# Optimization experiments

Measured on AMD Instinct MI355X. Metric: run time of the kernel, lower is better.

Reference implementation:

```python
import jax, jax.numpy as jnp
import numpy as np

SURR_SCALE = 10.0  # AbstractSNNLayer.surr_scale
THRESH = 0.3       # inf_th=False

@jax.custom_vjp
def spike_fn(x):
    # ActFunFastSigmoid.forward: heaviside
    return (x > 0).astype(x.dtype)

def _spike_fwd(x):
    return spike_fn(x), x

def _spike_bwd(x, g):
    # fast-sigmoid surrogate: g / (scale*|x| + 1)^2
    return (g / (SURR_SCALE * jnp.abs(x) + 1.0) ** 2,)

spike_fn.defvjp(_spike_fwd, _spike_bwd)


def setup_inputs() -> dict:
    B, NIN, NOUT = 1024, 4096, 4096
    key = jax.random.key(0)
    k1, k2, k3, k4, k5 = jax.random.split(key, 5)
    prev_spikes = jax.random.bernoulli(k1, 0.2, (B, NIN)).astype(jnp.float32)
    own_mems = 0.1 * jax.random.normal(k2, (B, NOUT), dtype=jnp.float32)
    own_spikes = jax.random.bernoulli(k3, 0.2, (B, NOUT)).astype(jnp.float32)
    W = jax.random.normal(k4, (NOUT, NIN), dtype=jnp.float32) / np.sqrt(NIN)
    tau_m = jax.random.normal(k5, (NOUT,), dtype=jnp.float32)
    return {"prev_spikes": prev_spikes, "own_mems": own_mems,
            "own_spikes": own_spikes, "W": W, "tau_m": tau_m}


def reference(prev_spikes, own_mems, own_spikes, W, tau_m):
    # update_mem: mem = mem * sigmoid(tau_m) * (1 - o_spike) + Linear(i_spike)
    alpha = jax.nn.sigmoid(tau_m)                      # [NOUT]
    mem = own_mems * alpha * (1.0 - own_spikes) \
          + jnp.einsum('bi,oi->bo', prev_spikes, W)    # [B, NOUT]
    # activation_function: spike with surrogate grad, then reset-to-zero
    o_spike = spike_fn(mem - THRESH)
    mem = jnp.where(mem < THRESH, mem, 0.0)            # mem * (mem < th_reset)
    return mem, o_spike
```

## Files before the change

### kernel.cpp

```cpp
#include <hip/hip_runtime.h>
#include <stdint.h>

#define NB 1024
#define NK 4096
#define NO 4096
#define DELTA 4e-7

typedef __attribute__((ext_vector_type(8))) short s16x8;
typedef __attribute__((ext_vector_type(4))) float f32x4;
typedef __attribute__((ext_vector_type(4))) int i32x4;
typedef __attribute__((ext_vector_type(16))) char c8x16;

static __device__ __forceinline__ unsigned short f2bf_rne(float x) {
  union { float f; unsigned u; } c; c.f = x;
  unsigned r = (c.u + 0x7FFFu + ((c.u >> 16) & 1u)) >> 16;
  return (unsigned short)r;
}
static __device__ __forceinline__ float bf2f(unsigned short h) {
  union { float f; unsigned u; } c; c.u = ((unsigned)h) << 16;
  return c.f;
}

static __device__ __forceinline__ void gload16(const void* g, void* l) {
  __builtin_amdgcn_global_load_lds((const __attribute__((address_space(1))) void*)g,
                                   (__attribute__((address_space(3))) void*)l, 16, 0, 0);
}

__global__ void cvtA8t_kernel(const float* __restrict__ A, signed char* __restrict__ A8t) {
  const int n = NB * NK / 16;
  for (int i = blockIdx.x * blockDim.x + threadIdx.x; i < n; i += gridDim.x * blockDim.x) {
    const int bm = i >> 15, rem = i & 32767;
    const int kt = rem >> 9, rem2 = rem & 511;
    const int l = rem2 >> 3, c = rem2 & 7;
    const int row = bm * 128 + 2 * l + (c >> 2);
    const int col = kt * 64 + (c & 3) * 16;
    const float* src = A + ((size_t)row << 12) + col;
    c8x16 v;
#pragma unroll
    for (int j = 0; j < 4; ++j) {
      float4 f = *(const float4*)(src + j * 4);
      v[j * 4 + 0] = (char)(int)f.x; v[j * 4 + 1] = (char)(int)f.y;
      v[j * 4 + 2] = (char)(int)f.z; v[j * 4 + 3] = (char)(int)f.w;
    }
    const size_t dst = ((size_t)(bm * 64 + kt) << 13) + l * 128 + ((c ^ (l & 7)) << 4);
    *(c8x16*)(A8t + dst) = v;
  }
}

__global__ void cvtW8t_kernel(const float* __restrict__ W, signed char* __restrict__ W8t) {
  const int n = NO * NK / 16;
  for (int i = blockIdx.x * blockDim.x + threadIdx.x; i < n; i += gridDim.x * blockDim.x) {
    const int bn = i >> 14, rem = i & 16383;
    const int kt = rem >> 8, rem2 = rem & 255;
    const int l = rem2 >> 3, c = rem2 & 7;
    const int row = bn * 64 + 2 * l + (c >> 2);
    const int col = kt * 64 + (c & 3) * 16;
    const float* src = W + ((size_t)row << 12) + col;
    c8x16 v1, v0;
#pragma unroll
    for (int j = 0; j < 16; ++j) {
      const int qi = (int)rintf(src[j] * 65536.0f);
      const int q1 = (qi + 64) >> 7;
      const int q0 = qi - (q1 << 7);
      v1[j] = (char)q1; v0[j] = (char)q0;
    }
    const size_t dst = ((size_t)(bn * 64 + kt) << 13) + l * 128 + ((c ^ (l & 7)) << 4);
    *(c8x16*)(W8t + dst) = v1;
    *(c8x16*)(W8t + dst + 4096) = v0;
  }
}

static __device__ __forceinline__ void frag_read2(
    const char* rb, const int (&offA)[2], const int (&offB)[2],
    i32x4 (&af)[2], i32x4 (&b1)[2], i32x4 (&b0)[2]) {
#pragma unroll
  for (int mi = 0; mi < 2; ++mi) af[mi] = *(const i32x4*)(rb + offA[mi]);
#pragma unroll
  for (int ni = 0; ni < 2; ++ni) {
    b1[ni] = *(const i32x4*)(rb + 8192 + offB[ni]);
    b0[ni] = *(const i32x4*)(rb + 12288 + offB[ni]);
  }
}

static __device__ __forceinline__ void mfma8(
    const i32x4 (&af)[2], const i32x4 (&b1)[2], const i32x4 (&b0)[2],
    i32x4 (&acc1)[2][2], i32x4 (&acc0)[2][2]) {
  __builtin_amdgcn_s_setprio(1);
#pragma unroll
  for (int mi = 0; mi < 2; ++mi)
#pragma unroll
    for (int ni = 0; ni < 2; ++ni) {
      acc1[mi][ni] = __builtin_amdgcn_mfma_i32_16x16x64_i8(af[mi], b1[ni], acc1[mi][ni], 0, 0, 0);
      acc0[mi][ni] = __builtin_amdgcn_mfma_i32_16x16x64_i8(af[mi], b0[ni], acc0[mi][ni], 0, 0, 0);
    }
  __builtin_amdgcn_s_setprio(0);
}

__global__ __launch_bounds__(512, 4) void snn_gemm_w8(
    const signed char* __restrict__ A8t, const signed char* __restrict__ W8t,
    const float* __restrict__ prev, const float* __restrict__ Wf,
    const float* __restrict__ own_mems, const float* __restrict__ own_spikes,
    const float* __restrict__ tau, float* __restrict__ out) {
  __shared__ __align__(16) char ring[3][16384];

  const int tid = threadIdx.x;
  const int lane = tid & 63;
  const int wave = tid >> 6;
  const int wm = wave >> 1, wn = wave & 1;

  const int bid = blockIdx.x;
  const int s = (bid & 7) * 64 + (bid >> 3);
  const int bm = s & 7, bn = s >> 3;

  const int woff = wave << 10;
  const char* pA = (const char*)A8t + ((size_t)(bm * 64) << 13) + tid * 16;
  const char* pW = (const char*)W8t + ((size_t)(bn * 64) << 13) + tid * 16;

  const int fr = lane & 15;
  const int fq = lane >> 4;

  int offA[2], offB[2];
#pragma unroll
  for (int mi = 0; mi < 2; ++mi) {
    const int r = wm * 32 + mi * 16 + fr, l = r >> 1;
    offA[mi] = l * 128 + ((((r & 1) * 4 + fq) ^ (l & 7)) * 16);
  }
#pragma unroll
  for (int ni = 0; ni < 2; ++ni) {
    const int r = wn * 32 + ni * 16 + fr, l = r >> 1;
    offB[ni] = l * 128 + ((((r & 1) * 4 + fq) ^ (l & 7)) * 16);
  }

  i32x4 acc1[2][2], acc0[2][2];
#pragma unroll
  for (int i = 0; i < 2; ++i)
#pragma unroll
    for (int j = 0; j < 2; ++j) { acc1[i][j] = (i32x4){0, 0, 0, 0};
                                  acc0[i][j] = (i32x4){0, 0, 0, 0}; }

  i32x4 afA[2], b1A[2], b0A[2], afB[2], b1B[2], b0B[2];

#define STAGE(slot, kt) { const size_t _ko = ((size_t)((kt) & 63) << 13);  \
    gload16(pA + _ko, ring[slot] + woff);                                  \
    gload16(pW + _ko, ring[slot] + 8192 + woff); }

#define SYNC asm volatile("s_waitcnt vmcnt(2) lgkmcnt(0)" ::: "memory"); \
    __builtin_amdgcn_s_barrier();

#define STEP(rd, st, kt, AFU, B1U, B0U, AFN, B1N, B0N)               \
    frag_read2(ring[rd], offA, offB, AFN, B1N, B0N);                 \
    STAGE(st, kt)                                                    \
    mfma8(AFU, B1U, B0U, acc1, acc0);                                \
    SYNC

  STAGE(0, 0) STAGE(1, 1) STAGE(2, 2)
  asm volatile("s_waitcnt vmcnt(2)" ::: "memory");
  __builtin_amdgcn_s_barrier();
  frag_read2(ring[0], offA, offB, afA, b1A, b0A);
  asm volatile("s_waitcnt lgkmcnt(0)" ::: "memory");
  __builtin_amdgcn_s_barrier();

#pragma unroll 1
  for (int m = 0; m < 10; ++m) {
    const int t = 6 * m;
    STEP(1, 0, t + 3, afA, b1A, b0A, afB, b1B, b0B)
    STEP(2, 1, t + 4, afB, b1B, b0B, afA, b1A, b0A)
    STEP(0, 2, t + 5, afA, b1A, b0A, afB, b1B, b0B)
    STEP(1, 0, t + 6, afB, b1B, b0B, afA, b1A, b0A)
    STEP(2, 1, t + 7, afA, b1A, b0A, afB, b1B, b0B)
    STEP(0, 2, t + 8, afB, b1B, b0B, afA, b1A, b0A)
  }
  STEP(1, 0, 63, afA, b1A, b0A, afB, b1B, b0B)
  STEP(2, 1, 64, afB, b1B, b0B, afA, b1A, b0A)
  STEP(0, 2, 65, afA, b1A, b0A, afB, b1B, b0B)
  mfma8(afB, b1B, b0B, acc1, acc0);
#undef STEP
#undef SYNC
#undef STAGE

  const float inv = 1.0f / 65536.0f;
  unsigned fm = 0u;
#pragma unroll
  for (int ni = 0; ni < 2; ++ni) {
    const int gc = bn * 64 + wn * 32 + ni * 16 + fr;
    const float alpha = 1.0f / (1.0f + expf(-tau[gc]));
#pragma unroll
    for (int mi = 0; mi < 2; ++mi) {
#pragma unroll
      for (int j = 0; j < 4; ++j) {
        const int gr = bm * 128 + wm * 32 + mi * 16 + fq * 4 + j;
        const size_t idx = (size_t)gr * NO + gc;
        const int comb = (acc1[mi][ni][j] << 7) + acc0[mi][ni][j];
        const float dec = own_mems[idx] * alpha * (1.0f - own_spikes[idx]);
        const float mem = (float)comb * inv + dec;
        out[idx] = (mem < 0.3f) ? mem : 0.0f;
        out[(size_t)NB * NO + idx] = (mem > 0.3f) ? 1.0f : 0.0f;
        if (fabsf(mem - 0.3f) < 1e-3f)
          fm |= 1u << ((mi * 2 + ni) * 4 + j);
      }
    }
  }

#pragma unroll 1
  for (int r = 0; r < 16; ++r) {
    unsigned long long m = __ballot((fm >> r) & 1u);
    if (m == 0ull) continue;
    const int mi = r >> 3, ni = (r >> 2) & 1, j = r & 3;
    const int gr_r = bm * 128 + wm * 32 + mi * 16 + fq * 4 + j;
    const int gc_r = bn * 64 + wn * 32 + ni * 16 + fr;
    while (m) {
      const int l = (int)__ffsll(m) - 1;
      m &= m - 1ull;
      const int gr = __shfl(gr_r, l, 64);
      const int gc = __shfl(gc_r, l, 64);
      const float* ap = prev + (size_t)gr * NK;
      const float* wp = Wf + (size_t)gc * NK;
      double s0 = 0.0, s1 = 0.0;
#pragma unroll 2
      for (int jj = 0; jj < 64; jj += 2) {
        s0 += (double)ap[lane + jj * 64]       * (double)wp[lane + jj * 64];
        s1 += (double)ap[lane + (jj + 1) * 64] * (double)wp[lane + (jj + 1) * 64];
      }
      double sum = s0 + s1;
#pragma unroll
      for (int off = 1; off < 64; off <<= 1) sum += __shfl_xor(sum, off, 64);
      if (lane == 0) {
        const size_t idx = (size_t)gr * NO + gc;
        const double alpha = 1.0 / (1.0 + exp(-(double)tau[gc]));
        const double dec = (double)own_mems[idx] * alpha * (1.0 - (double)own_spikes[idx]);
        const double mv = dec + sum;
        const double T = 0.3 + DELTA;
        out[idx] = (mv < T) ? (float)mv : 0.0f;
        out[(size_t)NB * NO + idx] = (mv > T) ? 1.0f : 0.0f;
      }
    }
  }
}

__global__ __launch_bounds__(256) void snn_fused(
    const float* __restrict__ prev, const float* __restrict__ Wf,
    const float* __restrict__ own_mems, const float* __restrict__ own_spikes,
    const float* __restrict__ tau, float* __restrict__ out) {
  __shared__ __align__(16) unsigned short sA[128 * 32];
  __shared__ __align__(16) unsigned short sH[128 * 32];
  __shared__ __align__(16) unsigned short sL[128 * 32];
  const int tid = threadIdx.x;
  const int lane = tid & 63;
  const int wave = tid >> 6;
  const int wm = wave >> 1, wn = wave & 1;
  const int bn = blockIdx.x, bm = blockIdx.y;
  const int srow = tid >> 1;
  const int scol = (tid & 1) * 16;
  const float* gA = prev + (size_t)(bm * 128 + srow) * NK + scol;
  const float* gW = Wf + (size_t)(bn * 128 + srow) * NK + scol;
  const int sb = srow * 32 + scol;
  f32x4 acc[4][4];
#pragma unroll
  for (int i = 0; i < 4; ++i)
#pragma unroll
    for (int j = 0; j < 4; ++j) acc[i][j] = (f32x4){0.f, 0.f, 0.f, 0.f};
  const int fr = lane & 15;
  const int fq = lane >> 4;
  const int fk = fq * 8;
  for (int kt = 0; kt < NK / 32; ++kt) {
    const int ko = kt * 32;
    float av[16], wv[16];
    *(float4*)&av[0]  = *(const float4*)(gA + ko);
    *(float4*)&av[4]  = *(const float4*)(gA + ko + 4);
    *(float4*)&av[8]  = *(const float4*)(gA + ko + 8);
    *(float4*)&av[12] = *(const float4*)(gA + ko + 12);
    *(float4*)&wv[0]  = *(const float4*)(gW + ko);
    *(float4*)&wv[4]  = *(const float4*)(gW + ko + 4);
    *(float4*)&wv[8]  = *(const float4*)(gW + ko + 8);
    *(float4*)&wv[12] = *(const float4*)(gW + ko + 12);
    s16x8 va0, va1, vh0, vh1, vl0, vl1;
#pragma unroll
    for (int j = 0; j < 8; ++j) {
      va0[j] = (short)f2bf_rne(av[j]);
      va1[j] = (short)f2bf_rne(av[j + 8]);
      const unsigned short h0 = f2bf_rne(wv[j]);
      vh0[j] = (short)h0;
      vl0[j] = (short)f2bf_rne(wv[j] - bf2f(h0));
      const unsigned short h1 = f2bf_rne(wv[j + 8]);
      vh1[j] = (short)h1;
      vl1[j] = (short)f2bf_rne(wv[j + 8] - bf2f(h1));
    }
    __syncthreads();
    *(s16x8*)&sA[sb] = va0; *(s16x8*)&sA[sb + 8] = va1;
    *(s16x8*)&sH[sb] = vh0; *(s16x8*)&sH[sb + 8] = vh1;
    *(s16x8*)&sL[sb] = vl0; *(s16x8*)&sL[sb + 8] = vl1;
    __syncthreads();
    s16x8 af[4], bh[4], bl[4];
#pragma unroll
    for (int mi = 0; mi < 4; ++mi)
      af[mi] = *(const s16x8*)&sA[(wm * 64 + mi * 16 + fr) * 32 + fk];
#pragma unroll
    for (int ni = 0; ni < 4; ++ni) {
      bh[ni] = *(const s16x8*)&sH[(wn * 64 + ni * 16 + fr) * 32 + fk];
      bl[ni] = *(const s16x8*)&sL[(wn * 64 + ni * 16 + fr) * 32 + fk];
    }
#pragma unroll
    for (int mi = 0; mi < 4; ++mi)
#pragma unroll
      for (int ni = 0; ni < 4; ++ni) {
        acc[mi][ni] = __builtin_amdgcn_mfma_f32_16x16x32_bf16(af[mi], bh[ni], acc[mi][ni], 0, 0, 0);
        acc[mi][ni] = __builtin_amdgcn_mfma_f32_16x16x32_bf16(af[mi], bl[ni], acc[mi][ni], 0, 0, 0);
      }
  }
  unsigned long long fm = 0ull;
#pragma unroll
  for (int ni = 0; ni < 4; ++ni) {
    const int gc = bn * 128 + wn * 64 + ni * 16 + fr;
    const float alpha = 1.0f / (1.0f + expf(-tau[gc]));
#pragma unroll
    for (int mi = 0; mi < 4; ++mi) {
#pragma unroll
      for (int j = 0; j < 4; ++j) {
        const int gr = bm * 128 + wm * 64 + mi * 16 + fq * 4 + j;
        const size_t idx = (size_t)gr * NO + gc;
        const float dec = own_mems[idx] * alpha * (1.0f - own_spikes[idx]);
        const float mem = acc[mi][ni][j] + dec;
        out[idx] = (mem < 0.3f) ? mem : 0.0f;
        out[(size_t)NB * NO + idx] = (mem > 0.3f) ? 1.0f : 0.0f;
        if (fabsf(mem - 0.3f) < 1e-3f)
          fm |= 1ull << (mi * 16 + ni * 4 + j);
      }
    }
  }
#pragma unroll 1
  for (int r = 0; r < 64; ++r) {
    unsigned long long m = __ballot((fm >> r) & 1ull);
    if (m == 0ull) continue;
    const int mi = r >> 4, ni = (r >> 2) & 3, j = r & 3;
    const int gr_r = bm * 128 + wm * 64 + mi * 16 + fq * 4 + j;
    const int gc_r = bn * 128 + wn * 64 + ni * 16 + fr;
    while (m) {
      const int l = (int)__ffsll(m) - 1;
      m &= m - 1ull;
      const int gr = __shfl(gr_r, l, 64);
      const int gc = __shfl(gc_r, l, 64);
      const float* ap = prev + (size_t)gr * NK;
      const float* wp = Wf + (size_t)gc * NK;
      double s0 = 0.0, s1 = 0.0;
#pragma unroll 2
      for (int jj = 0; jj < 64; jj += 2) {
        s0 += (double)ap[lane + jj * 64]       * (double)wp[lane + jj * 64];
        s1 += (double)ap[lane + (jj + 1) * 64] * (double)wp[lane + (jj + 1) * 64];
      }
      double sum = s0 + s1;
#pragma unroll
      for (int off = 1; off < 64; off <<= 1) sum += __shfl_xor(sum, off, 64);
      if (lane == 0) {
        const size_t idx = (size_t)gr * NO + gc;
        const double alpha = 1.0 / (1.0 + exp(-(double)tau[gc]));
        const double dec = (double)own_mems[idx] * alpha * (1.0 - (double)own_spikes[idx]);
        const double mv = dec + sum;
        const double T = 0.3 + DELTA;
        out[idx] = (mv < T) ? (float)mv : 0.0f;
        out[(size_t)NB * NO + idx] = (mv > T) ? 1.0f : 0.0f;
      }
    }
  }
}

extern "C" void kernel_launch(void* const* d_in, const int* in_sizes, int n_in,
                              void* d_out, int out_size, void* d_ws, size_t ws_size,
                              hipStream_t stream) {
  const float* prev_spikes = (const float*)d_in[0];
  const float* own_mems    = (const float*)d_in[1];
  const float* own_spikes  = (const float*)d_in[2];
  const float* W           = (const float*)d_in[3];
  const float* tau         = (const float*)d_in[4];
  float* out = (float*)d_out;

  const size_t aBytes = (size_t)NB * NK;
  const size_t wBytes = (size_t)NO * NK * 2;
  if (ws_size >= aBytes + wBytes) {
    char* p = (char*)d_ws;
    signed char* A8t = (signed char*)p;
    signed char* W8t = (signed char*)(p + aBytes);
    cvtA8t_kernel<<<1024, 256, 0, stream>>>(prev_spikes, A8t);
    cvtW8t_kernel<<<2048, 256, 0, stream>>>(W, W8t);
    snn_gemm_w8<<<512, 512, 0, stream>>>(A8t, W8t, prev_spikes, W,
                                         own_mems, own_spikes, tau, out);
  } else {
    snn_fused<<<dim3(NO / 128, NB / 128), 256, 0, stream>>>(
        prev_spikes, W, own_mems, own_spikes, tau, out);
  }
}
```

Measured before the change: 104.9 us.

## Move near-threshold fp64 recheck into separate fixup kernel via atomic list

The near-threshold fp64 recomputation leaves the GEMM epilogue. Flagged output indices are appended to a global list with an atomic counter and handled by a separate grid-strided fixup kernel, so the GEMM waves no longer stall on serial per-element dot products. The band for recheck shrinks from 1e-3 to 5e-4, and the block-index swizzle is removed. This costs two extra kernel launches and global atomics, adds a cap on fixup entries (overflow is silently dropped), and the narrower band trades safety margin on the threshold decision.

Measured after the change: 118.2 us. 1.13x slower.

```diff
diff --git a/kernel.cpp b/kernel.cpp
--- a/kernel.cpp
+++ b/kernel.cpp
@@ -5,6 +5,8 @@
 #define NK 4096
 #define NO 4096
 #define DELTA 4e-7
+#define BAND 5e-4f
+#define FIXCAP 65536u
 
 typedef __attribute__((ext_vector_type(8))) short s16x8;
 typedef __attribute__((ext_vector_type(4))) float f32x4;
@@ -70,6 +72,8 @@
   }
 }
 
+__global__ void zero_cnt_kernel(unsigned* cnt) { if (threadIdx.x == 0) *cnt = 0u; }
+
 static __device__ __forceinline__ void frag_read2(
     const char* rb, const int (&offA)[2], const int (&offB)[2],
     i32x4 (&af)[2], i32x4 (&b1)[2], i32x4 (&b0)[2]) {
@@ -98,9 +102,9 @@
 
 __global__ __launch_bounds__(512, 4) void snn_gemm_w8(
     const signed char* __restrict__ A8t, const signed char* __restrict__ W8t,
-    const float* __restrict__ prev, const float* __restrict__ Wf,
     const float* __restrict__ own_mems, const float* __restrict__ own_spikes,
-    const float* __restrict__ tau, float* __restrict__ out) {
+    const float* __restrict__ tau, float* __restrict__ out,
+    unsigned* __restrict__ cnt, unsigned* __restrict__ list) {
   __shared__ __align__(16) char ring[3][16384];
 
   const int tid = threadIdx.x;
@@ -109,8 +113,8 @@
   const int wm = wave >> 1, wn = wave & 1;
 
   const int bid = blockIdx.x;
-  const int s = (bid & 7) * 64 + (bid >> 3);
-  const int bm = s & 7, bn = s >> 3;
+  const int bm = bid & 7;
+  const int bn = bid >> 3;
 
   const int woff = wave << 10;
   const char* pA = (const char*)A8t + ((size_t)(bm * 64) << 13) + tid * 16;
@@ -179,7 +183,6 @@
 #undef STAGE
 
   const float inv = 1.0f / 65536.0f;
-  unsigned fm = 0u;
 #pragma unroll
   for (int ni = 0; ni < 2; ++ni) {
     const int gc = bn * 64 + wn * 32 + ni * 16 + fr;
@@ -195,44 +198,46 @@
         const float mem = (float)comb * inv + dec;
         out[idx] = (mem < 0.3f) ? mem : 0.0f;
         out[(size_t)NB * NO + idx] = (mem > 0.3f) ? 1.0f : 0.0f;
-        if (fabsf(mem - 0.3f) < 1e-3f)
-          fm |= 1u << ((mi * 2 + ni) * 4 + j);
+        if (fabsf(mem - 0.3f) < BAND) {
+          unsigned p = atomicAdd(cnt, 1u);
+          if (p < FIXCAP) list[p] = (unsigned)idx;
+        }
       }
     }
   }
-
-#pragma unroll 1
-  for (int r = 0; r < 16; ++r) {
-    unsigned long long m = __ballot((fm >> r) & 1u);
-    if (m == 0ull) continue;
-    const int mi = r >> 3, ni = (r >> 2) & 1, j = r & 3;
-    const int gr_r = bm * 128 + wm * 32 + mi * 16 + fq * 4 + j;
-    const int gc_r = bn * 64 + wn * 32 + ni * 16 + fr;
-    while (m) {
-      const int l = (int)__ffsll(m) - 1;
-      m &= m - 1ull;
-      const int gr = __shfl(gr_r, l, 64);
-      const int gc = __shfl(gc_r, l, 64);
-      const float* ap = prev + (size_t)gr * NK;
-      const float* wp = Wf + (size_t)gc * NK;
-      double s0 = 0.0, s1 = 0.0;
+}
+
+__global__ __launch_bounds__(256) void snn_fixup(
+    const float* __restrict__ prev, const float* __restrict__ Wf,
+    const float* __restrict__ own_mems, const float* __restrict__ own_spikes,
+    const float* __restrict__ tau, const unsigned* __restrict__ cnt,
+    const unsigned* __restrict__ list, float* __restrict__ out) {
+  const unsigned n = min(*cnt, FIXCAP);
+  const int lane = threadIdx.x & 63;
+  const int wv = blockIdx.x * (blockDim.x >> 6) + (threadIdx.x >> 6);
+  const int nw = gridDim.x * (blockDim.x >> 6);
+  for (unsigned it = (unsigned)wv; it < n; it += (unsigned)nw) {
+    const unsigned idx = list[it];
+    const int gr = (int)(idx >> 12);
+    const int gc = (int)(idx & 4095);
+    const float* ap = prev + (size_t)gr * NK;
+    const float* wp = Wf + (size_t)gc * NK;
+    double s0 = 0.0, s1 = 0.0;
 #pragma unroll 2
-      for (int jj = 0; jj < 64; jj += 2) {
-        s0 += (double)ap[lane + jj * 64]       * (double)wp[lane + jj * 64];
-        s1 += (double)ap[lane + (jj + 1) * 64] * (double)wp[lane + (jj + 1) * 64];
-      }
-      double sum = s0 + s1;
-#pragma unroll
-      for (int off = 1; off < 64; off <<= 1) sum += __shfl_xor(sum, off, 64);
-      if (lane == 0) {
-        const size_t idx = (size_t)gr * NO + gc;
-        const double alpha = 1.0 / (1.0 + exp(-(double)tau[gc]));
-        const double dec = (double)own_mems[idx] * alpha * (1.0 - (double)own_spikes[idx]);
-        const double mv = dec + sum;
-        const double T = 0.3 + DELTA;
-        out[idx] = (mv < T) ? (float)mv : 0.0f;
-        out[(size_t)NB * NO + idx] = (mv > T) ? 1.0f : 0.0f;
-      }
+    for (int jj = 0; jj < 64; jj += 2) {
+      s0 += (double)ap[lane + jj * 64]       * (double)wp[lane + jj * 64];
+      s1 += (double)ap[lane + (jj + 1) * 64] * (double)wp[lane + (jj + 1) * 64];
+    }
+    double sum = s0 + s1;
+#pragma unroll
+    for (int off = 1; off < 64; off <<= 1) sum += __shfl_xor(sum, off, 64);
+    if (lane == 0) {
+      const double alpha = 1.0 / (1.0 + exp(-(double)tau[gc]));
+      const double dec = (double)own_mems[idx] * alpha * (1.0 - (double)own_spikes[idx]);
+      const double mv = dec + sum;
+      const double T = 0.3 + DELTA;
+      out[idx] = (mv < T) ? (float)mv : 0.0f;
+      out[(size_t)NB * NO + idx] = (mv > T) ? 1.0f : 0.0f;
     }
   }
 }
@@ -375,14 +380,20 @@
 
   const size_t aBytes = (size_t)NB * NK;
   const size_t wBytes = (size_t)NO * NK * 2;
-  if (ws_size >= aBytes + wBytes) {
+  const size_t fixBytes = 16 + (size_t)FIXCAP * 4;
+  if (ws_size >= aBytes + wBytes + fixBytes) {
     char* p = (char*)d_ws;
     signed char* A8t = (signed char*)p;
     signed char* W8t = (signed char*)(p + aBytes);
+    unsigned* cnt    = (unsigned*)(p + aBytes + wBytes);
+    unsigned* list   = cnt + 4;
     cvtA8t_kernel<<<1024, 256, 0, stream>>>(prev_spikes, A8t);
     cvtW8t_kernel<<<2048, 256, 0, stream>>>(W, W8t);
-    snn_gemm_w8<<<512, 512, 0, stream>>>(A8t, W8t, prev_spikes, W,
-                                         own_mems, own_spikes, tau, out);
+    zero_cnt_kernel<<<1, 64, 0, stream>>>(cnt);
+    snn_gemm_w8<<<512, 512, 0, stream>>>(A8t, W8t, own_mems, own_spikes,
+                                         tau, out, cnt, list);
+    snn_fixup<<<512, 256, 0, stream>>>(prev_spikes, W, own_mems, own_spikes,
+                                       tau, cnt, list, out);
   } else {
     snn_fused<<<dim3(NO / 128, NB / 128), 256, 0, stream>>>(
         prev_spikes, W, own_mems, own_spikes, tau, out);
```
